# Kernel optimization log

Measured on AMD Instinct MI355X. Metric: run time of the kernel, lower is better.

## Reference

```python
import jax, jax.numpy as jnp
import numpy as np

PYR = 30000
PV, SST, VIP, NGC = 3000, 2250, 1500, 750
DT = 0.5          # dt_ms
E_L, E_E, E_I = 0.0, 3.0, -0.5
TAU_NIC, TAU_MUS = 50.0, 200.0   # ACh receptor trace time constants (ms)
V_RESET = 0.0


def _sparse_gaussian(key, n_out, n_in, conn, mean, std, no_autapse=False):
    km, kw = jax.random.split(key)
    mask = jax.random.uniform(km, (n_out, n_in)) < conn
    w = mean + std * jax.random.normal(kw, (n_out, n_in))
    w = jnp.where(mask, w, 0.0)
    if no_autapse:
        w = w * (1.0 - jnp.eye(n_out, dtype=w.dtype))
    return w.astype(jnp.float32)


def _hetero(key, mean, n, cv):
    v = mean * (1.0 + cv * jax.random.normal(key, (n,)))
    return jnp.clip(v, 0.5 * mean, 1.5 * mean).astype(jnp.float32)


def setup_inputs() -> dict:
    key = jax.random.key(0)
    ks = list(jax.random.split(key, 40))
    inp = {}
    # synaptic conductances computed by parent column (non-negative)
    inp['pv_g_exc'] = (0.1 * jax.random.uniform(ks[0], (PV,))).astype(jnp.float32)
    inp['pv_g_inh'] = (0.05 * jax.random.uniform(ks[1], (PV,))).astype(jnp.float32)
    inp['sst_g_exc'] = (0.1 * jax.random.uniform(ks[2], (SST,))).astype(jnp.float32)
    inp['sst_g_inh'] = (0.05 * jax.random.uniform(ks[3], (SST,))).astype(jnp.float32)
    inp['vip_g_exc_from_pyr'] = (0.1 * jax.random.uniform(ks[4], (VIP,))).astype(jnp.float32)
    inp['vip_g_inh'] = jnp.zeros((VIP,), jnp.float32)
    inp['ngc_g_exc_from_pyr'] = (0.1 * jax.random.uniform(ks[5], (NGC,))).astype(jnp.float32)
    inp['ngc_g_inh'] = jnp.zeros((NGC,), jnp.float32)
    inp['feedforward_excitation'] = (0.1 * jax.random.uniform(ks[6], (PV,))).astype(jnp.float32)
    inp['long_range_excitation'] = jax.random.uniform(ks[7], (PYR,)).astype(jnp.float32)
    inp['ach_spikes'] = jax.random.uniform(ks[8], (1,)).astype(jnp.float32)
    # sparse Gaussian long-range / gap-junction weights
    inp['w_lr_vip'] = _sparse_gaussian(ks[9], VIP, PYR, 0.4, 0.001, 0.0005)
    inp['w_lr_ngc'] = _sparse_gaussian(ks[10], NGC, PYR, 0.3, 0.0008, 0.0004)
    inp['w_pv_gap'] = _sparse_gaussian(ks[11], PV, PV, 0.5, 0.004, 0.001, no_autapse=True)
    # delayed PV membrane buffer + ACh receptor traces (module state)
    inp['prev_pv_mem'] = (0.2 * jax.random.uniform(ks[12], (PV,))).astype(jnp.float32)
    inp['nic_trace'] = (0.1 * jax.random.uniform(ks[13], (VIP,))).astype(jnp.float32)
    inp['mus_trace'] = (0.1 * jax.random.uniform(ks[14], (NGC,))).astype(jnp.float32)
    # heterogeneous per-neuron parameters and membrane/adaptation state
    inp['pv_g_L'] = _hetero(ks[15], 0.1, PV, 0.08)
    inp['pv_tau_mem'] = _hetero(ks[16], 5.0, PV, 0.1)
    inp['pv_v_th'] = _hetero(ks[17], 0.75, PV, 0.06)
    inp['pv_adapt_inc'] = _hetero(ks[18], 0.1, PV, 0.1)
    inp['pv_v'] = (0.3 * jax.random.uniform(ks[19], (PV,))).astype(jnp.float32)
    inp['pv_adapt'] = (0.05 * jax.random.uniform(ks[20], (PV,))).astype(jnp.float32)
    inp['sst_g_L'] = _hetero(ks[21], 0.05, SST, 0.1)
    inp['sst_tau_mem'] = _hetero(ks[22], 15.0, SST, 0.1)
    inp['sst_v_th'] = _hetero(ks[23], 0.8, SST, 0.06)
    inp['sst_adapt_inc'] = _hetero(ks[24], 0.1, SST, 0.1)
    inp['sst_v'] = (0.3 * jax.random.uniform(ks[25], (SST,))).astype(jnp.float32)
    inp['sst_adapt'] = (0.05 * jax.random.uniform(ks[26], (SST,))).astype(jnp.float32)
    inp['vip_g_L'] = _hetero(ks[27], 0.05, VIP, 0.1)
    inp['vip_tau_mem'] = _hetero(ks[28], 10.0, VIP, 0.1)
    inp['vip_v_th'] = _hetero(ks[29], 0.95, VIP, 0.06)
    inp['vip_adapt_inc'] = _hetero(ks[30], 0.12, VIP, 0.1)
    inp['vip_v'] = (0.3 * jax.random.uniform(ks[31], (VIP,))).astype(jnp.float32)
    inp['vip_adapt'] = (0.05 * jax.random.uniform(ks[32], (VIP,))).astype(jnp.float32)
    inp['ngc_g_L'] = _hetero(ks[33], 0.05, NGC, 0.1)
    inp['ngc_tau_mem'] = _hetero(ks[34], 15.0, NGC, 0.1)
    inp['ngc_v_th'] = _hetero(ks[35], 0.8, NGC, 0.06)
    inp['ngc_adapt_inc'] = _hetero(ks[36], 0.3, NGC, 0.1)
    inp['ngc_v'] = (0.3 * jax.random.uniform(ks[37], (NGC,))).astype(jnp.float32)
    inp['ngc_adapt'] = (0.05 * jax.random.uniform(ks[38], (NGC,))).astype(jnp.float32)
    return inp


def _lif(v, adapt, g_exc, g_inh, i_extra, g_L, tau_mem, v_th, adapt_inc):
    # conductance-based LIF, single Euler step of dt = DT ms
    C = g_L * tau_mem  # membrane capacitance: tau_mem = C / g_L
    I = g_L * (E_L - v) + g_exc * (E_E - v) + g_inh * (E_I - v) + i_extra
    v_new = v + DT * I / C
    spk = (v_new >= v_th + adapt).astype(v.dtype)
    v_out = jnp.where(spk > 0, V_RESET, v_new)
    return spk, v_out


def reference(pv_g_exc, pv_g_inh, sst_g_exc, sst_g_inh,
              vip_g_exc_from_pyr, vip_g_inh, ngc_g_exc_from_pyr, ngc_g_inh,
              feedforward_excitation, long_range_excitation, ach_spikes,
              w_lr_vip, w_lr_ngc, w_pv_gap, prev_pv_mem, nic_trace, mus_trace,
              pv_g_L, pv_tau_mem, pv_v_th, pv_adapt_inc, pv_v, pv_adapt,
              sst_g_L, sst_tau_mem, sst_v_th, sst_adapt_inc, sst_v, sst_adapt,
              vip_g_L, vip_tau_mem, vip_v_th, vip_adapt_inc, vip_v, vip_adapt,
              ngc_g_L, ngc_tau_mem, ngc_v_th, ngc_adapt_inc, ngc_v, ngc_adapt):
    # optional thalamic feedforward drive directly to PV
    pv_gE = pv_g_exc + feedforward_excitation
    # long-range top-down input routed to VIP / NGC via sparse weights
    vip_lr = jnp.matmul(w_lr_vip, long_range_excitation)   # [VIP]
    ngc_lr = jnp.matmul(w_lr_ngc, long_range_excitation)   # [NGC]
    # ACh receptor traces (exponential synapses driven by NB spikes)
    nic = nic_trace * jnp.exp(-DT / TAU_NIC) + ach_spikes  # broadcast scalar spike
    mus = mus_trace * jnp.exp(-DT / TAU_MUS) + ach_spikes
    vip_gE = vip_g_exc_from_pyr + vip_lr + nic * 0.25
    ngc_gE = ngc_g_exc_from_pyr + ngc_lr + mus * 0.2
    # gap-junction (electrical) coupling among PV cells, using 1-step delayed membrane
    pv_gap = jnp.matmul(w_pv_gap, prev_pv_mem) - prev_pv_mem * jnp.sum(w_pv_gap, axis=1)
    # integrate the four interneuron populations
    pv_spk, pv_mem = _lif(pv_v, pv_adapt, pv_gE, pv_g_inh, pv_gap,
                          pv_g_L, pv_tau_mem, pv_v_th, pv_adapt_inc)
    sst_spk, sst_mem = _lif(sst_v, sst_adapt, sst_g_exc, sst_g_inh, 0.0,
                            sst_g_L, sst_tau_mem, sst_v_th, sst_adapt_inc)
    vip_spk, vip_mem = _lif(vip_v, vip_adapt, vip_gE, vip_g_inh, 0.0,
                            vip_g_L, vip_tau_mem, vip_v_th, vip_adapt_inc)
    ngc_spk, ngc_mem = _lif(ngc_v, ngc_adapt, ngc_gE, ngc_g_inh, 0.0,
                            ngc_g_L, ngc_tau_mem, ngc_v_th, ngc_adapt_inc)
    return (pv_spk, sst_spk, vip_spk, ngc_spk, pv_mem, sst_mem, vip_mem, ngc_mem)
```

## Files before the change

### kernel.cpp

```cpp
#include <hip/hip_runtime.h>
#include <math.h>

#define N_PYR 30000
#define N_PV  3000
#define N_SST 2250
#define N_VIP 1500
#define N_NGC 750
#define N_BIG (N_VIP + N_NGC)

#define DT    0.5f
#define E_E   3.0f
#define E_I   (-0.5f)
#define NIC_DECAY 0.9900498337491681f
#define MUS_DECAY 0.9975031223974601f

#define BIG_QUADS   ((N_BIG + 3) / 4)
#define N_CHUNKS    4
#define KCHUNK      (N_PYR / N_CHUNKS)
#define BIG_BLOCKS  (BIG_QUADS * N_CHUNKS)
#define GAP_BLOCKS  (N_PV / 4)

#define WS_GAP (N_CHUNKS * N_BIG)

__device__ __forceinline__ float dot4(const float4 w, const float4 x) {
    return w.x * x.x + w.y * x.y + w.z * x.z + w.w * x.w;
}
__device__ __forceinline__ float sum4(const float4 w) {
    return w.x + w.y + w.z + w.w;
}

__global__ __launch_bounds__(256) void matvec_k(
    const float* __restrict__ w_vip, const float* __restrict__ w_ngc,
    const float* __restrict__ w_gap, const float* __restrict__ lre,
    const float* __restrict__ prev, float* __restrict__ ws)
{
    const int b = blockIdx.x;
    const int t = threadIdx.x;

    const float4* __restrict__ w0;
    const float4* __restrict__ w1;
    const float4* __restrict__ w2;
    const float4* __restrict__ w3;
    const float4* __restrict__ xv;
    int n4, r0, dst, nv;
    bool is_gap = false;

    if (b < BIG_BLOCKS) {
        const int q     = b >> 2;
        const int chunk = b & 3;
        r0 = 4 * q;
        nv = (N_BIG - r0 < 4) ? (N_BIG - r0) : 4;
        const float* bp[4];
        #pragma unroll
        for (int k = 0; k < 4; ++k) {
            int rr = r0 + k; if (rr > N_BIG - 1) rr = N_BIG - 1;
            const float* base = (rr < N_VIP)
                ? (w_vip + (size_t)rr * N_PYR)
                : (w_ngc + (size_t)(rr - N_VIP) * N_PYR);
            bp[k] = base + chunk * KCHUNK;
        }
        w0 = (const float4*)bp[0]; w1 = (const float4*)bp[1];
        w2 = (const float4*)bp[2]; w3 = (const float4*)bp[3];
        xv = (const float4*)(lre + chunk * KCHUNK);
        n4 = KCHUNK / 4;
        dst = chunk * N_BIG + r0;
    } else {
        const int g = b - BIG_BLOCKS;
        r0 = 4 * g;
        nv = 4;
        w0 = (const float4*)(w_gap + (size_t)r0 * N_PV);
        w1 = (const float4*)(w_gap + (size_t)(r0 + 1) * N_PV);
        w2 = (const float4*)(w_gap + (size_t)(r0 + 2) * N_PV);
        w3 = (const float4*)(w_gap + (size_t)(r0 + 3) * N_PV);
        xv = (const float4*)prev;
        n4 = N_PV / 4;
        is_gap = true;
        dst = WS_GAP + r0;
    }

    float a0 = 0.f, a1 = 0.f, a2 = 0.f, a3 = 0.f;
    float s0 = 0.f, s1 = 0.f, s2 = 0.f, s3 = 0.f;

    int i = t;
    for (; i + 256 < n4; i += 512) {
        const float4 xA = xv[i];
        const float4 xB = xv[i + 256];
        const float4 wA0 = w0[i];       const float4 wA1 = w1[i];
        const float4 wA2 = w2[i];       const float4 wA3 = w3[i];
        const float4 wB0 = w0[i + 256]; const float4 wB1 = w1[i + 256];
        const float4 wB2 = w2[i + 256]; const float4 wB3 = w3[i + 256];
        a0 += dot4(wA0, xA) + dot4(wB0, xB);
        a1 += dot4(wA1, xA) + dot4(wB1, xB);
        a2 += dot4(wA2, xA) + dot4(wB2, xB);
        a3 += dot4(wA3, xA) + dot4(wB3, xB);
        if (is_gap) {
            s0 += sum4(wA0) + sum4(wB0);
            s1 += sum4(wA1) + sum4(wB1);
            s2 += sum4(wA2) + sum4(wB2);
            s3 += sum4(wA3) + sum4(wB3);
        }
    }
    if (i < n4) {
        const float4 xA = xv[i];
        const float4 wA0 = w0[i]; const float4 wA1 = w1[i];
        const float4 wA2 = w2[i]; const float4 wA3 = w3[i];
        a0 += dot4(wA0, xA);
        a1 += dot4(wA1, xA);
        a2 += dot4(wA2, xA);
        a3 += dot4(wA3, xA);
        if (is_gap) {
            s0 += sum4(wA0); s1 += sum4(wA1);
            s2 += sum4(wA2); s3 += sum4(wA3);
        }
    }

    #pragma unroll
    for (int off = 32; off > 0; off >>= 1) {
        a0 += __shfl_down(a0, off, 64);
        a1 += __shfl_down(a1, off, 64);
        a2 += __shfl_down(a2, off, 64);
        a3 += __shfl_down(a3, off, 64);
        s0 += __shfl_down(s0, off, 64);
        s1 += __shfl_down(s1, off, 64);
        s2 += __shfl_down(s2, off, 64);
        s3 += __shfl_down(s3, off, 64);
    }

    __shared__ float sm[4][8];
    const int wid = t >> 6, lane = t & 63;
    if (lane == 0) {
        sm[wid][0] = a0; sm[wid][1] = a1; sm[wid][2] = a2; sm[wid][3] = a3;
        sm[wid][4] = s0; sm[wid][5] = s1; sm[wid][6] = s2; sm[wid][7] = s3;
    }
    __syncthreads();
    if (t < nv) {
        float a = sm[0][t] + sm[1][t] + sm[2][t] + sm[3][t];
        if (is_gap) {
            const float rs = sm[0][4 + t] + sm[1][4 + t] + sm[2][4 + t] + sm[3][4 + t];
            a -= prev[r0 + t] * rs;
        }
        ws[dst + t] = a;
    }
}

struct LifArgs {
    const float *pv_g_exc, *pv_g_inh, *sst_g_exc, *sst_g_inh;
    const float *vip_g_exc, *vip_g_inh, *ngc_g_exc, *ngc_g_inh;
    const float *ffe, *ach, *nic, *mus;
    const float *pv_gL, *pv_tau, *pv_vth, *pv_v, *pv_ad;
    const float *sst_gL, *sst_tau, *sst_vth, *sst_v, *sst_ad;
    const float *vip_gL, *vip_tau, *vip_vth, *vip_v, *vip_ad;
    const float *ngc_gL, *ngc_tau, *ngc_vth, *ngc_v, *ngc_ad;
    const float *ws;
    float *out;
};

__device__ __forceinline__ void lif_step(
    float v, float adapt, float gE, float gI, float iex,
    float gL, float tau, float vth, float& spk, float& vout)
{
    const float C = gL * tau;
    const float I = gL * (0.0f - v) + gE * (E_E - v) + gI * (E_I - v) + iex;
    const float v_new = v + DT * I / C;
    spk = (v_new >= vth + adapt) ? 1.0f : 0.0f;
    vout = (spk > 0.0f) ? 0.0f : v_new;
}

__global__ __launch_bounds__(256) void lif_k(LifArgs a)
{
    const int i = blockIdx.x * 256 + threadIdx.x;
    const int total = N_PV + N_SST + N_VIP + N_NGC;
    if (i >= total) return;

    float spk, vout;
    if (i < N_PV) {
        const int j = i;
        const float gE = a.pv_g_exc[j] + a.ffe[j];
        const float iex = a.ws[WS_GAP + j];
        lif_step(a.pv_v[j], a.pv_ad[j], gE, a.pv_g_inh[j], iex,
                 a.pv_gL[j], a.pv_tau[j], a.pv_vth[j], spk, vout);
        a.out[j] = spk;
        a.out[total + j] = vout;
    } else if (i < N_PV + N_SST) {
        const int j = i - N_PV;
        lif_step(a.sst_v[j], a.sst_ad[j], a.sst_g_exc[j], a.sst_g_inh[j], 0.0f,
                 a.sst_gL[j], a.sst_tau[j], a.sst_vth[j], spk, vout);
        a.out[N_PV + j] = spk;
        a.out[total + N_PV + j] = vout;
    } else if (i < N_PV + N_SST + N_VIP) {
        const int j = i - N_PV - N_SST;
        const float nic = a.nic[j] * NIC_DECAY + a.ach[0];
        const float lr = a.ws[j] + a.ws[N_BIG + j]
                       + a.ws[2 * N_BIG + j] + a.ws[3 * N_BIG + j];
        const float gE = a.vip_g_exc[j] + lr + nic * 0.25f;
        lif_step(a.vip_v[j], a.vip_ad[j], gE, a.vip_g_inh[j], 0.0f,
                 a.vip_gL[j], a.vip_tau[j], a.vip_vth[j], spk, vout);
        a.out[N_PV + N_SST + j] = spk;
        a.out[total + N_PV + N_SST + j] = vout;
    } else {
        const int j = i - N_PV - N_SST - N_VIP;
        const float mus = a.mus[j] * MUS_DECAY + a.ach[0];
        const int r = N_VIP + j;
        const float lr = a.ws[r] + a.ws[N_BIG + r]
                       + a.ws[2 * N_BIG + r] + a.ws[3 * N_BIG + r];
        const float gE = a.ngc_g_exc[j] + lr + mus * 0.2f;
        lif_step(a.ngc_v[j], a.ngc_ad[j], gE, a.ngc_g_inh[j], 0.0f,
                 a.ngc_gL[j], a.ngc_tau[j], a.ngc_vth[j], spk, vout);
        a.out[N_PV + N_SST + N_VIP + j] = spk;
        a.out[total + N_PV + N_SST + N_VIP + j] = vout;
    }
}

extern "C" void kernel_launch(void* const* d_in, const int* in_sizes, int n_in,
                              void* d_out, int out_size, void* d_ws, size_t ws_size,
                              hipStream_t stream) {
    const float* pv_g_exc  = (const float*)d_in[0];
    const float* pv_g_inh  = (const float*)d_in[1];
    const float* sst_g_exc = (const float*)d_in[2];
    const float* sst_g_inh = (const float*)d_in[3];
    const float* vip_g_exc = (const float*)d_in[4];
    const float* vip_g_inh = (const float*)d_in[5];
    const float* ngc_g_exc = (const float*)d_in[6];
    const float* ngc_g_inh = (const float*)d_in[7];
    const float* ffe       = (const float*)d_in[8];
    const float* lre       = (const float*)d_in[9];
    const float* ach       = (const float*)d_in[10];
    const float* w_lr_vip  = (const float*)d_in[11];
    const float* w_lr_ngc  = (const float*)d_in[12];
    const float* w_pv_gap  = (const float*)d_in[13];
    const float* prev_pv   = (const float*)d_in[14];
    const float* nic_trace = (const float*)d_in[15];
    const float* mus_trace = (const float*)d_in[16];

    const float* pv_gL   = (const float*)d_in[17];
    const float* pv_tau  = (const float*)d_in[18];
    const float* pv_vth  = (const float*)d_in[19];
    const float* pv_v    = (const float*)d_in[21];
    const float* pv_ad   = (const float*)d_in[22];

    const float* sst_gL   = (const float*)d_in[23];
    const float* sst_tau  = (const float*)d_in[24];
    const float* sst_vth  = (const float*)d_in[25];
    const float* sst_v    = (const float*)d_in[27];
    const float* sst_ad   = (const float*)d_in[28];

    const float* vip_gL   = (const float*)d_in[29];
    const float* vip_tau  = (const float*)d_in[30];
    const float* vip_vth  = (const float*)d_in[31];
    const float* vip_v    = (const float*)d_in[33];
    const float* vip_ad   = (const float*)d_in[34];

    const float* ngc_gL   = (const float*)d_in[35];
    const float* ngc_tau  = (const float*)d_in[36];
    const float* ngc_vth  = (const float*)d_in[37];
    const float* ngc_v    = (const float*)d_in[39];
    const float* ngc_ad   = (const float*)d_in[40];

    float* ws  = (float*)d_ws;
    float* out = (float*)d_out;

    matvec_k<<<BIG_BLOCKS + GAP_BLOCKS, 256, 0, stream>>>(
        w_lr_vip, w_lr_ngc, w_pv_gap, lre, prev_pv, ws);

    LifArgs a;
    a.pv_g_exc = pv_g_exc; a.pv_g_inh = pv_g_inh;
    a.sst_g_exc = sst_g_exc; a.sst_g_inh = sst_g_inh;
    a.vip_g_exc = vip_g_exc; a.vip_g_inh = vip_g_inh;
    a.ngc_g_exc = ngc_g_exc; a.ngc_g_inh = ngc_g_inh;
    a.ffe = ffe; a.ach = ach; a.nic = nic_trace; a.mus = mus_trace;
    a.pv_gL = pv_gL; a.pv_tau = pv_tau; a.pv_vth = pv_vth;
    a.pv_v = pv_v; a.pv_ad = pv_ad;
    a.sst_gL = sst_gL; a.sst_tau = sst_tau; a.sst_vth = sst_vth;
    a.sst_v = sst_v; a.sst_ad = sst_ad;
    a.vip_gL = vip_gL; a.vip_tau = vip_tau; a.vip_vth = vip_vth;
    a.vip_v = vip_v; a.vip_ad = vip_ad;
    a.ngc_gL = ngc_gL; a.ngc_tau = ngc_tau; a.ngc_vth = ngc_vth;
    a.ngc_v = ngc_v; a.ngc_ad = ngc_ad;
    a.ws = ws; a.out = out;

    lif_k<<<(N_PV + N_SST + N_VIP + N_NGC + 255) / 256, 256, 0, stream>>>(a);
}
```

Baseline: 52.23 us.

## Stream weight rows through LDS with async global_load_lds pipeline per wave

Restructures the matvec so each wave handles one weight row and streams it into LDS using global_load_lds with a 4-deep software pipeline governed by explicit s_waitcnt vmcnt, while the x vector is staged in shared memory once per block. The aim is to keep more memory requests in flight and shift the weight traffic onto the async LDS path instead of register loads. It drops the cross-wave shared-memory reduction but relies on hand-tuned page counts and tail lanes and on an ordering assumption between the vmcnt waits and the LDS reads, which is fragile.

```diff
diff --git a/kernel.cpp b/kernel.cpp
--- a/kernel.cpp
+++ b/kernel.cpp
@@ -14,19 +14,32 @@
 #define NIC_DECAY 0.9900498337491681f
 #define MUS_DECAY 0.9975031223974601f
 
-#define BIG_QUADS   ((N_BIG + 3) / 4)
 #define N_CHUNKS    4
 #define KCHUNK      (N_PYR / N_CHUNKS)
+#define BIG_QUADS   ((N_BIG + 3) / 4)
 #define BIG_BLOCKS  (BIG_QUADS * N_CHUNKS)
 #define GAP_BLOCKS  (N_PV / 4)
 
+#define NP_BIG   30
+#define TL_BIG   19
+#define NP_GAP   12
+#define TL_GAP   46
+
 #define WS_GAP (N_CHUNKS * N_BIG)
+
+#define WAITVM(N) asm volatile("s_waitcnt vmcnt(" #N ")" ::: "memory")
 
 __device__ __forceinline__ float dot4(const float4 w, const float4 x) {
     return w.x * x.x + w.y * x.y + w.z * x.z + w.w * x.w;
 }
 __device__ __forceinline__ float sum4(const float4 w) {
     return w.x + w.y + w.z + w.w;
+}
+
+__device__ __forceinline__ void load_lds16(const void* gsrc, void* lds_dst) {
+    __builtin_amdgcn_global_load_lds(
+        (const __attribute__((address_space(1))) void*)gsrc,
+        (__attribute__((address_space(3))) void*)lds_dst, 16, 0, 0);
 }
 
 __global__ __launch_bounds__(256) void matvec_k(
@@ -34,113 +47,99 @@
     const float* __restrict__ w_gap, const float* __restrict__ lre,
     const float* __restrict__ prev, float* __restrict__ ws)
 {
+    __shared__ float4 xs[KCHUNK / 4];
+    __shared__ float4 wsl[4][512];
+
     const int b = blockIdx.x;
     const int t = threadIdx.x;
-
-    const float4* __restrict__ w0;
-    const float4* __restrict__ w1;
-    const float4* __restrict__ w2;
-    const float4* __restrict__ w3;
-    const float4* __restrict__ xv;
-    int n4, r0, dst, nv;
-    bool is_gap = false;
+    const int wv = t >> 6;
+    const int lane = t & 63;
+
+    const float* wrow;
+    const float* xsrc;
+    int xn4, NP, tailL, r, dst;
+    bool is_gap, valid = true;
 
     if (b < BIG_BLOCKS) {
-        const int q     = b >> 2;
-        const int chunk = b & 3;
-        r0 = 4 * q;
-        nv = (N_BIG - r0 < 4) ? (N_BIG - r0) : 4;
-        const float* bp[4];
-        #pragma unroll
-        for (int k = 0; k < 4; ++k) {
-            int rr = r0 + k; if (rr > N_BIG - 1) rr = N_BIG - 1;
-            const float* base = (rr < N_VIP)
-                ? (w_vip + (size_t)rr * N_PYR)
-                : (w_ngc + (size_t)(rr - N_VIP) * N_PYR);
-            bp[k] = base + chunk * KCHUNK;
-        }
-        w0 = (const float4*)bp[0]; w1 = (const float4*)bp[1];
-        w2 = (const float4*)bp[2]; w3 = (const float4*)bp[3];
-        xv = (const float4*)(lre + chunk * KCHUNK);
-        n4 = KCHUNK / 4;
-        dst = chunk * N_BIG + r0;
+        const int q = b >> 2, chunk = b & 3;
+        r = 4 * q + wv;
+        if (r >= N_BIG) { r = N_BIG - 1; valid = false; }
+        const float* base = (r < N_VIP)
+            ? (w_vip + (size_t)r * N_PYR)
+            : (w_ngc + (size_t)(r - N_VIP) * N_PYR);
+        wrow = base + chunk * KCHUNK;
+        xsrc = lre + chunk * KCHUNK;
+        xn4 = KCHUNK / 4;
+        NP = NP_BIG; tailL = TL_BIG;
+        dst = chunk * N_BIG + r;
+        is_gap = false;
     } else {
         const int g = b - BIG_BLOCKS;
-        r0 = 4 * g;
-        nv = 4;
-        w0 = (const float4*)(w_gap + (size_t)r0 * N_PV);
-        w1 = (const float4*)(w_gap + (size_t)(r0 + 1) * N_PV);
-        w2 = (const float4*)(w_gap + (size_t)(r0 + 2) * N_PV);
-        w3 = (const float4*)(w_gap + (size_t)(r0 + 3) * N_PV);
-        xv = (const float4*)prev;
-        n4 = N_PV / 4;
+        r = 4 * g + wv;
+        wrow = w_gap + (size_t)r * N_PV;
+        xsrc = prev;
+        xn4 = N_PV / 4;
+        NP = NP_GAP; tailL = TL_GAP;
+        dst = WS_GAP + r;
         is_gap = true;
-        dst = WS_GAP + r0;
-    }
-
-    float a0 = 0.f, a1 = 0.f, a2 = 0.f, a3 = 0.f;
-    float s0 = 0.f, s1 = 0.f, s2 = 0.f, s3 = 0.f;
-
-    int i = t;
-    for (; i + 256 < n4; i += 512) {
-        const float4 xA = xv[i];
-        const float4 xB = xv[i + 256];
-        const float4 wA0 = w0[i];       const float4 wA1 = w1[i];
-        const float4 wA2 = w2[i];       const float4 wA3 = w3[i];
-        const float4 wB0 = w0[i + 256]; const float4 wB1 = w1[i + 256];
-        const float4 wB2 = w2[i + 256]; const float4 wB3 = w3[i + 256];
-        a0 += dot4(wA0, xA) + dot4(wB0, xB);
-        a1 += dot4(wA1, xA) + dot4(wB1, xB);
-        a2 += dot4(wA2, xA) + dot4(wB2, xB);
-        a3 += dot4(wA3, xA) + dot4(wB3, xB);
-        if (is_gap) {
-            s0 += sum4(wA0) + sum4(wB0);
-            s1 += sum4(wA1) + sum4(wB1);
-            s2 += sum4(wA2) + sum4(wB2);
-            s3 += sum4(wA3) + sum4(wB3);
-        }
-    }
-    if (i < n4) {
-        const float4 xA = xv[i];
-        const float4 wA0 = w0[i]; const float4 wA1 = w1[i];
-        const float4 wA2 = w2[i]; const float4 wA3 = w3[i];
-        a0 += dot4(wA0, xA);
-        a1 += dot4(wA1, xA);
-        a2 += dot4(wA2, xA);
-        a3 += dot4(wA3, xA);
-        if (is_gap) {
-            s0 += sum4(wA0); s1 += sum4(wA1);
-            s2 += sum4(wA2); s3 += sum4(wA3);
-        }
-    }
+    }
+
+    {
+        const float4* xv4 = (const float4*)xsrc;
+        for (int i = t; i < xn4; i += 256) xs[i] = xv4[i];
+    }
+
+    const char* gbase = (const char*)wrow + lane * 16;
+    char* lbase = (char*)&wsl[wv][0];
+    #pragma unroll
+    for (int p = 0; p < 4; ++p)
+        load_lds16(gbase + p * 1024, lbase + p * 1024);
+
+    __syncthreads();
+
+    float acc = 0.0f, sac = 0.0f;
+
+    #define ISSUE(P) do {                                                   \
+        const int p_ = (P);                                                 \
+        const char* s_ = gbase + p_ * 1024;                                 \
+        if (p_ == NP - 1 && lane >= tailL) s_ = (const char*)wrow;          \
+        load_lds16(s_, lbase + (p_ & 7) * 1024);                            \
+    } while (0)
+
+    #define CONSUME(P, NL) do {                                             \
+        const int p_ = (P);                                                 \
+        if (lane < (NL)) {                                                  \
+            const float4 wq = wsl[wv][(p_ & 7) * 64 + lane];                \
+            const float4 xq = xs[p_ * 64 + lane];                           \
+            acc += dot4(wq, xq);                                            \
+            if (is_gap) sac += sum4(wq);                                    \
+        }                                                                   \
+    } while (0)
+
+    for (int p = 0; p < NP - 4; ++p) {
+        ISSUE(p + 4);
+        WAITVM(4);
+        CONSUME(p, 64);
+    }
+    WAITVM(3); CONSUME(NP - 4, 64);
+    WAITVM(2); CONSUME(NP - 3, 64);
+    WAITVM(1); CONSUME(NP - 2, 64);
+    WAITVM(0); CONSUME(NP - 1, tailL);
 
     #pragma unroll
     for (int off = 32; off > 0; off >>= 1) {
-        a0 += __shfl_down(a0, off, 64);
-        a1 += __shfl_down(a1, off, 64);
-        a2 += __shfl_down(a2, off, 64);
-        a3 += __shfl_down(a3, off, 64);
-        s0 += __shfl_down(s0, off, 64);
-        s1 += __shfl_down(s1, off, 64);
-        s2 += __shfl_down(s2, off, 64);
-        s3 += __shfl_down(s3, off, 64);
-    }
-
-    __shared__ float sm[4][8];
-    const int wid = t >> 6, lane = t & 63;
-    if (lane == 0) {
-        sm[wid][0] = a0; sm[wid][1] = a1; sm[wid][2] = a2; sm[wid][3] = a3;
-        sm[wid][4] = s0; sm[wid][5] = s1; sm[wid][6] = s2; sm[wid][7] = s3;
-    }
-    __syncthreads();
-    if (t < nv) {
-        float a = sm[0][t] + sm[1][t] + sm[2][t] + sm[3][t];
-        if (is_gap) {
-            const float rs = sm[0][4 + t] + sm[1][4 + t] + sm[2][4 + t] + sm[3][4 + t];
-            a -= prev[r0 + t] * rs;
-        }
-        ws[dst + t] = a;
-    }
+        acc += __shfl_down(acc, off, 64);
+        sac += __shfl_down(sac, off, 64);
+    }
+
+    if (lane == 0 && valid) {
+        float res = acc;
+        if (is_gap) res = acc - prev[r] * sac;
+        ws[dst] = res;
+    }
+
+    #undef ISSUE
+    #undef CONSUME
 }
 
 struct LifArgs {
```

Measured after the change: 110.6 us. 2.12x slower.
